# Optimization experiments

Measured on AMD Instinct MI355X. Metric: run time of the kernel, lower is better.

## Reference

```python
import jax, jax.numpy as jnp
import numpy as np

S, B, D, H, E, NUM_TASKS = 2048, 16, 1024, 256, 4, 8
EXPERT_DIMS = jnp.array([256.0, 512.0, 1024.0, 2048.0], dtype=jnp.float32)
EXPERT_COST_EXPONENT = 1.0


def setup_inputs() -> dict:
    key = jax.random.key(0)
    ks = jax.random.split(key, 8)
    s = 1.0 / np.sqrt(H)
    return {
        "prev_layer_output": jax.random.normal(ks[0], (S, B, D), dtype=jnp.float32),
        "task_ids": jax.random.randint(ks[1], (S, B), 0, NUM_TASKS),
        "W_ih": jax.random.uniform(ks[2], (3 * H, D), minval=-s, maxval=s, dtype=jnp.float32),
        "W_hh": jax.random.uniform(ks[3], (3 * H, H), minval=-s, maxval=s, dtype=jnp.float32),
        "b_ih": jax.random.uniform(ks[4], (3 * H,), minval=-s, maxval=s, dtype=jnp.float32),
        "b_hh": jax.random.uniform(ks[5], (3 * H,), minval=-s, maxval=s, dtype=jnp.float32),
        "W_out": jax.random.uniform(ks[6], (E, H), minval=-s, maxval=s, dtype=jnp.float32),
        "b_out": jax.random.uniform(ks[7], (E,), minval=-s, maxval=s, dtype=jnp.float32),
    }


def _gru(x, W_ih, W_hh, b_ih, b_hh):
    # x: (S, B, D); precompute input projections once (big GEMM)
    xp = jnp.einsum('sbd,gd->sbg', x, W_ih) + b_ih  # (S, B, 3H)

    def step(h, xp_t):
        hp = h @ W_hh.T + b_hh                       # (B, 3H)
        xr, xz, xn = jnp.split(xp_t, 3, axis=-1)     # PyTorch gate order: r, z, n
        hr, hz, hn = jnp.split(hp, 3, axis=-1)
        r = jax.nn.sigmoid(xr + hr)
        z = jax.nn.sigmoid(xz + hz)
        n = jnp.tanh(xn + r * hn)
        h_new = (1.0 - z) * n + z * h
        return h_new, h_new

    h0 = jnp.zeros((x.shape[1], W_hh.shape[1]), dtype=x.dtype)
    _, hs = jax.lax.scan(step, h0, xp)
    return hs  # (S, B, H)


def reference(prev_layer_output, task_ids, W_ih, W_hh, b_ih, b_hh, W_out, b_out):
    hs = _gru(prev_layer_output, W_ih, W_hh, b_ih, b_hh)
    logits = jax.nn.relu(hs) @ W_out.T + b_out       # (S, B, E)
    raw_router_output = jax.nn.softmax(logits, axis=-1)
    router_output = raw_router_output                # no dropout branches active
    indices = jnp.broadcast_to(jnp.arange(E, dtype=jnp.int64), (S, B, E))

    routing_costs = EXPERT_DIMS ** EXPERT_COST_EXPONENT
    expert_usage_loss = jnp.einsum('sbe,e->sb', raw_router_output, routing_costs)

    # per-task masked mean == segment_sum / segment_count (fused scatter-reduce)
    flat_ids = task_ids.reshape(-1)
    flat_loss = expert_usage_loss.reshape(-1)
    sums = jax.ops.segment_sum(flat_loss, flat_ids, num_segments=NUM_TASKS)
    counts = jax.ops.segment_sum(jnp.ones_like(flat_loss), flat_ids, num_segments=NUM_TASKS)
    task_expert_usage_losses = sums / counts         # (NUM_TASKS,)

    return raw_router_output, router_output, indices, task_expert_usage_losses
```

## Files before the change

kernel.cpp:

```cpp
#include <hip/hip_runtime.h>

#define NSTEP 2048

typedef __attribute__((ext_vector_type(8))) short short8;
typedef __attribute__((ext_vector_type(4))) float f32x4;
typedef __attribute__((ext_vector_type(4))) int i32x4;

static __device__ __forceinline__ unsigned short f2bf(float f){
  unsigned u = __builtin_bit_cast(unsigned, f);
  u += 0x7FFFu + ((u >> 16) & 1u);
  return (unsigned short)(u >> 16);
}

__global__ __launch_bounds__(256,1)
void cvt_bf16_k(const float* __restrict__ in, unsigned short* __restrict__ out, int n4){
  int i = blockIdx.x*256 + threadIdx.x;
  if (i < n4){
    f32x4 v = *(const f32x4*)(in + (size_t)i*4);
    ushort4 o; o.x=f2bf(v.x); o.y=f2bf(v.y); o.z=f2bf(v.z); o.w=f2bf(v.w);
    *(ushort4*)(out + (size_t)i*4) = o;
  }
}

__global__ __launch_bounds__(256,1)
void gemm_xp_k(const float* __restrict__ X, const unsigned short* __restrict__ Wb,
               const float* __restrict__ bih, const float* __restrict__ bhh,
               float* __restrict__ XP){
  __shared__ __align__(16) unsigned short sA[128*40];
  __shared__ __align__(16) unsigned short sB[128*40];
  const float NL2E  = -1.4426950408889634f;
  const float NL2E2 = -2.8853900817779268f;
  int bid = blockIdx.x;
  int xcd = bid & 7, loc = bid >> 3;
  int mt = xcd*32 + loc/6;
  int nt = loc % 6;
  int m0 = mt*128, n0 = nt*128;
  int tid = threadIdx.x;
  int lane = tid & 63, wave = tid >> 6;
  int wm = wave >> 1, wn = wave & 1;
  int rA = lane & 15, kg = lane >> 4;
  f32x4 acc[4][4] = {};
  for (int k0 = 0; k0 < 1024; k0 += 32){
    __syncthreads();
    #pragma unroll
    for (int q = 0; q < 4; q++){
      int idx = tid + q*256;
      int r = idx >> 3, c4 = idx & 7;
      f32x4 v = *(const f32x4*)(X + (size_t)(m0+r)*1024 + k0 + c4*4);
      ushort4 o; o.x=f2bf(v.x); o.y=f2bf(v.y); o.z=f2bf(v.z); o.w=f2bf(v.w);
      *(ushort4*)&sA[r*40 + c4*4] = o;
    }
    #pragma unroll
    for (int q = 0; q < 2; q++){
      int idx = tid + q*256;
      int n = idx >> 2, c8 = idx & 3;
      uint4 v = *(const uint4*)(Wb + (size_t)(n0+n)*1024 + k0 + c8*8);
      *(uint4*)&sB[n*40 + c8*8] = v;
    }
    __syncthreads();
    short8 af[4], bf[4];
    #pragma unroll
    for (int i=0;i<4;i++) af[i] = *(const short8*)&sA[(wm*64 + 16*i + rA)*40 + kg*8];
    #pragma unroll
    for (int j=0;j<4;j++) bf[j] = *(const short8*)&sB[(wn*64 + 16*j + rA)*40 + kg*8];
    #pragma unroll
    for (int i=0;i<4;i++)
      #pragma unroll
      for (int j=0;j<4;j++)
        acc[i][j] = __builtin_amdgcn_mfma_f32_16x16x32_bf16(af[i], bf[j], acc[i][j], 0, 0, 0);
  }
  #pragma unroll
  for (int i=0;i<4;i++){
    int rb = m0 + wm*64 + 16*i + kg*4;
    #pragma unroll
    for (int j=0;j<4;j++){
      int cc = n0 + wn*64 + 16*j + rA;
      float bv = bih[cc] + bhh[cc];
      float sc = (cc < 512) ? NL2E : NL2E2;
      #pragma unroll
      for (int rg=0;rg<4;rg++)
        XP[(size_t)(rb+rg)*768 + cc] = (acc[i][j][rg] + bv) * sc;
    }
  }
}

__global__ __launch_bounds__(512,2)
void gru_k(const float* __restrict__ xp, const float* __restrict__ Whh,
           char* __restrict__ hs8){
  int b = blockIdx.x;
  int tid = threadIdx.x;
  int wave = tid >> 6, lane = tid & 63;
  int rA = lane & 15, kg = lane >> 4;
  int ua = 32*wave + rA;
  __shared__ __align__(16) char h_q[2][256];

  const float NL2E  = -1.4426950408889634f;
  const float NL2E2 = -2.8853900817779268f;

  i32x4 bw[3][2][4];
  float dsc[3][2];
  #pragma unroll
  for (int g=0; g<3; g++){
    #pragma unroll
    for (int hh=0; hh<2; hh++){
      const float* rp = Whh + (size_t)(g*256 + 32*wave + hh*16 + rA)*256 + kg*16;
      float mx = 0.f;
      #pragma unroll
      for (int kk=0; kk<4; kk++)
        #pragma unroll
        for (int j=0; j<16; j++)
          mx = fmaxf(mx, fabsf(rp[kk*64 + j]));
      mx = fmaxf(mx, __shfl_xor(mx, 16, 64));
      mx = fmaxf(mx, __shfl_xor(mx, 32, 64));
      mx = fmaxf(mx, 1e-20f);
      float s = 127.f / mx;
      float fold = (g == 2) ? NL2E2 : NL2E;
      dsc[g][hh] = mx * (1.f/(127.f*127.f)) * fold;
      #pragma unroll
      for (int kk=0; kk<4; kk++){
        i32x4 v;
        #pragma unroll
        for (int q=0; q<4; q++){
          const float* pp = rp + kk*64 + q*4;
          int q0 = __float2int_rn(pp[0]*s) & 255;
          int q1 = __float2int_rn(pp[1]*s) & 255;
          int q2 = __float2int_rn(pp[2]*s) & 255;
          int q3 = __float2int_rn(pp[3]*s) & 255;
          v[q] = q0 | (q1<<8) | (q2<<16) | (q3<<24);
        }
        bw[g][hh][kk] = v;
      }
    }
  }
  if (tid < 256) h_q[0][tid] = 0;
  __syncthreads();

  float xa[2][3], xb[2][3];
  {
    const float* q0 = xp + (size_t)b*768;
    const float* q1 = xp + (size_t)(16 + b)*768;
    #pragma unroll
    for (int g=0; g<3; g++){
      xa[0][g] = q0[g*256 + ua];  xb[0][g] = q0[g*256 + ua + 16];
      xa[1][g] = q1[g*256 + ua];  xb[1][g] = q1[g*256 + ua + 16];
    }
  }
  float ha = 0.f, hb = 0.f;
  const float* pA = xp + (size_t)(2*16 + b)*768 + ua;
  char* ph = hs8 + (size_t)b*256 + ua;

#define GRU_HALF(half, DO_REFILL)                                                        \
  {                                                                                      \
    i32x4 a[4];                                                                          \
    _Pragma("unroll")                                                                    \
    for (int kk=0; kk<4; kk++)                                                           \
      a[kk] = *(const i32x4*)&h_q[half][kk*64 + kg*16];                                  \
    i32x4 a00={}, a01={}, a10={}, a11={}, a20={}, a21={};                                \
    __builtin_amdgcn_s_setprio(1);                                                       \
    _Pragma("unroll")                                                                    \
    for (int kk=0; kk<4; kk++){                                                          \
      a00 = __builtin_amdgcn_mfma_i32_16x16x64_i8(a[kk], bw[0][0][kk], a00, 0,0,0);      \
      a01 = __builtin_amdgcn_mfma_i32_16x16x64_i8(a[kk], bw[0][1][kk], a01, 0,0,0);      \
      a10 = __builtin_amdgcn_mfma_i32_16x16x64_i8(a[kk], bw[1][0][kk], a10, 0,0,0);      \
      a11 = __builtin_amdgcn_mfma_i32_16x16x64_i8(a[kk], bw[1][1][kk], a11, 0,0,0);      \
      a20 = __builtin_amdgcn_mfma_i32_16x16x64_i8(a[kk], bw[2][0][kk], a20, 0,0,0);      \
      a21 = __builtin_amdgcn_mfma_i32_16x16x64_i8(a[kk], bw[2][1][kk], a21, 0,0,0);      \
    }                                                                                    \
    __builtin_amdgcn_s_setprio(0);                                                       \
    float ra = __builtin_amdgcn_rcpf(1.f + __builtin_amdgcn_exp2f(fmaf((float)a00[0], dsc[0][0], xa[half][0]))); \
    float rb = __builtin_amdgcn_rcpf(1.f + __builtin_amdgcn_exp2f(fmaf((float)a01[0], dsc[0][1], xb[half][0]))); \
    float za = __builtin_amdgcn_rcpf(1.f + __builtin_amdgcn_exp2f(fmaf((float)a10[0], dsc[1][0], xa[half][1]))); \
    float zb = __builtin_amdgcn_rcpf(1.f + __builtin_amdgcn_exp2f(fmaf((float)a11[0], dsc[1][1], xb[half][1]))); \
    float na = fmaf(2.f, __builtin_amdgcn_rcpf(1.f + __builtin_amdgcn_exp2f(             \
                 fmaf(ra, (float)a20[0]*dsc[2][0], xa[half][2]))), -1.f);                \
    float nb = fmaf(2.f, __builtin_amdgcn_rcpf(1.f + __builtin_amdgcn_exp2f(             \
                 fmaf(rb, (float)a21[0]*dsc[2][1], xb[half][2]))), -1.f);                \
    ha = fmaf(za, ha - na, na);                                                          \
    hb = fmaf(zb, hb - nb, nb);                                                          \
    int qa = __float2int_rn(ha*127.f), qb = __float2int_rn(hb*127.f);                    \
    if (kg == 0){                                                                        \
      h_q[half^1][ua]    = (char)qa;                                                     \
      h_q[half^1][ua+16] = (char)qb;                                                     \
    }                                                                                    \
    if (kg == 1){                                                                        \
      ph[0]  = (char)qa;                                                                 \
      ph[16] = (char)qb;                                                                 \
    }                                                                                    \
    ph += 4096;                                                                          \
    if (DO_REFILL){                                                                      \
      xa[half][0] = pA[0];  xa[half][1] = pA[256]; xa[half][2] = pA[512];                \
      xb[half][0] = pA[16]; xb[half][1] = pA[272]; xb[half][2] = pA[528];                \
      pA += 12288;                                                                       \
    }                                                                                    \
    __builtin_amdgcn_sched_barrier(0);                                                   \
    asm volatile("s_waitcnt lgkmcnt(0)" ::: "memory");                                   \
    __builtin_amdgcn_s_barrier();                                                        \
    __builtin_amdgcn_sched_barrier(0);                                                   \
  }

  for (int t = 0; t < NSTEP-2; t += 2){
    GRU_HALF(0, 1)
    GRU_HALF(1, 1)
  }
  GRU_HALF(0, 0)
  GRU_HALF(1, 0)
#undef GRU_HALF
}

__global__ __launch_bounds__(256,1)
void head_k(const char* __restrict__ hs8, const float* __restrict__ Wout,
            const float* __restrict__ bout, const int* __restrict__ task,
            float* __restrict__ out, float* __restrict__ sums, float* __restrict__ counts){
  __shared__ float sW[1024];
  __shared__ float sbin[8], scnt[8];
  int tid = threadIdx.x;
  for (int i = tid; i < 1024; i += 256) sW[i] = Wout[i] * (1.f/127.f);
  if (tid < 8){ sbin[tid] = 0.f; scnt[tid] = 0.f; }
  __syncthreads();
  int rowi = blockIdx.x*256 + tid;
  const uint4* hp = (const uint4*)(hs8 + (size_t)rowi*256);
  float l0 = bout[0], l1 = bout[1], l2 = bout[2], l3 = bout[3];
  #pragma unroll 4
  for (int c = 0; c < 16; c++){
    uint4 v = hp[c];
    uint arr[4] = {v.x, v.y, v.z, v.w};
    #pragma unroll
    for (int q = 0; q < 4; q++){
      uint w = arr[q];
      int k = c*16 + q*4;
      float h0 = (float)max((int)(char)(w      ), 0);
      float h1 = (float)max((int)(char)(w >>  8), 0);
      float h2 = (float)max((int)(char)(w >> 16), 0);
      float h3 = (float)max((int)(w) >> 24,       0);
      l0 = fmaf(h0, sW[k],     l0); l0 = fmaf(h1, sW[k+1],     l0);
      l0 = fmaf(h2, sW[k+2],   l0); l0 = fmaf(h3, sW[k+3],     l0);
      l1 = fmaf(h0, sW[256+k], l1); l1 = fmaf(h1, sW[257+k],   l1);
      l1 = fmaf(h2, sW[258+k], l1); l1 = fmaf(h3, sW[259+k],   l1);
      l2 = fmaf(h0, sW[512+k], l2); l2 = fmaf(h1, sW[513+k],   l2);
      l2 = fmaf(h2, sW[514+k], l2); l2 = fmaf(h3, sW[515+k],   l2);
      l3 = fmaf(h0, sW[768+k], l3); l3 = fmaf(h1, sW[769+k],   l3);
      l3 = fmaf(h2, sW[770+k], l3); l3 = fmaf(h3, sW[771+k],   l3);
    }
  }
  float mx = fmaxf(fmaxf(l0,l1), fmaxf(l2,l3));
  float e0 = __expf(l0-mx), e1 = __expf(l1-mx), e2 = __expf(l2-mx), e3 = __expf(l3-mx);
  float inv = 1.f/(e0+e1+e2+e3);
  float p0 = e0*inv, p1 = e1*inv, p2 = e2*inv, p3 = e3*inv;
  size_t o = (size_t)rowi*4;
  out[o+0]=p0; out[o+1]=p1; out[o+2]=p2; out[o+3]=p3;
  out[131072+o+0]=p0; out[131072+o+1]=p1; out[131072+o+2]=p2; out[131072+o+3]=p3;
  out[262144+o+0]=0.f; out[262144+o+1]=1.f; out[262144+o+2]=2.f; out[262144+o+3]=3.f;
  float loss = 256.f*p0 + 512.f*p1 + 1024.f*p2 + 2048.f*p3;
  int tk = task[rowi] & 7;
  atomicAdd(&sbin[tk], loss);
  atomicAdd(&scnt[tk], 1.f);
  __syncthreads();
  if (tid < 8){
    atomicAdd(&sums[tid], sbin[tid]);
    atomicAdd(&counts[tid], scnt[tid]);
  }
}

__global__ void fin_k(const float* __restrict__ sums, const float* __restrict__ counts,
                      float* __restrict__ o3){
  int i = threadIdx.x;
  if (i < 8){ float c = counts[i]; o3[i] = c > 0.f ? sums[i]/c : 0.f; }
}

extern "C" void kernel_launch(void* const* d_in, const int* in_sizes, int n_in,
                              void* d_out, int out_size, void* d_ws, size_t ws_size,
                              hipStream_t stream){
  const float* x    = (const float*)d_in[0];
  const int*   task = (const int*)d_in[1];
  const float* Wih  = (const float*)d_in[2];
  const float* Whh  = (const float*)d_in[3];
  const float* bih  = (const float*)d_in[4];
  const float* bhh  = (const float*)d_in[5];
  const float* Wout = (const float*)d_in[6];
  const float* bout = (const float*)d_in[7];
  float* out = (float*)d_out;
  char* ws = (char*)d_ws;
  unsigned short* wih_bf = (unsigned short*)ws;
  float* xp    = (float*)(ws + 1572864);
  char* hs8    = (char*)(ws + 102236160);
  float* sums  = (float*)(ws + 111149056);
  float* counts= (float*)(ws + 111149088);

  hipMemsetAsync(sums, 0, 64, stream);

  cvt_bf16_k<<<768, 256, 0, stream>>>(Wih, wih_bf, 196608);
  gemm_xp_k<<<1536, 256, 0, stream>>>(x, wih_bf, bih, bhh, xp);
  gru_k<<<16, 512, 0, stream>>>(xp, Whh, hs8);
  head_k<<<128, 256, 0, stream>>>(hs8, Wout, bout, task, out, sums, counts);
  fin_k<<<1, 64, 0, stream>>>(sums, counts, out + 393216);
}
```

Before: 1.378 ms.

## Overlap input-projection GEMM with GRU recurrence via fused persistent kernel and flags

Result: slower. 1.685 ms (+22.2%).

```diff
diff --git a/kernel.cpp b/kernel.cpp
--- a/kernel.cpp
+++ b/kernel.cpp
@@ -23,17 +23,15 @@
 }
 
 __global__ __launch_bounds__(256,1)
-void gemm_xp_k(const float* __restrict__ X, const unsigned short* __restrict__ Wb,
-               const float* __restrict__ bih, const float* __restrict__ bhh,
-               float* __restrict__ XP){
+void gemm_head_k(const float* __restrict__ X, const unsigned short* __restrict__ Wb,
+                 const float* __restrict__ bih, const float* __restrict__ bhh,
+                 float* __restrict__ XP){
   __shared__ __align__(16) unsigned short sA[128*40];
   __shared__ __align__(16) unsigned short sB[128*40];
   const float NL2E  = -1.4426950408889634f;
   const float NL2E2 = -2.8853900817779268f;
   int bid = blockIdx.x;
-  int xcd = bid & 7, loc = bid >> 3;
-  int mt = xcd*32 + loc/6;
-  int nt = loc % 6;
+  int mt = bid / 6, nt = bid % 6;
   int m0 = mt*128, n0 = nt*128;
   int tid = threadIdx.x;
   int lane = tid & 63, wave = tid >> 6;
@@ -85,17 +83,81 @@
 }
 
 __global__ __launch_bounds__(512,2)
-void gru_k(const float* __restrict__ xp, const float* __restrict__ Whh,
-           char* __restrict__ hs8){
-  int b = blockIdx.x;
-  int tid = threadIdx.x;
-  int wave = tid >> 6, lane = tid & 63;
-  int rA = lane & 15, kg = lane >> 4;
-  int ua = 32*wave + rA;
+void fused_k(const float* __restrict__ xp_c, float* __restrict__ XP,
+             const float* __restrict__ X, const unsigned short* __restrict__ Wb,
+             const float* __restrict__ bih, const float* __restrict__ bhh,
+             const float* __restrict__ Whh, char* __restrict__ hs8,
+             int* prog, int* wgcnt, int* done){
+  __shared__ __align__(16) unsigned short sA[128*40];
+  __shared__ __align__(16) unsigned short sB[128*40];
   __shared__ __align__(16) char h_q[2][256];
 
   const float NL2E  = -1.4426950408889634f;
   const float NL2E2 = -2.8853900817779268f;
+  int tid = threadIdx.x;
+  int lane = tid & 63, wave = tid >> 6;
+  int rA = lane & 15, kg = lane >> 4;
+
+  if (blockIdx.x >= 16){
+    int gbid = blockIdx.x - 16;
+    int mt = 32 + gbid / 6, nt = gbid % 6;
+    int m0 = mt*128, n0 = nt*128;
+    int wm = wave >> 1, wn = wave & 1;
+    f32x4 acc[2][4] = {};
+    for (int k0 = 0; k0 < 1024; k0 += 32){
+      __syncthreads();
+      #pragma unroll
+      for (int q = 0; q < 2; q++){
+        int idx = tid + q*512;
+        int r = idx >> 3, c4 = idx & 7;
+        f32x4 v = *(const f32x4*)(X + (size_t)(m0+r)*1024 + k0 + c4*4);
+        ushort4 o; o.x=f2bf(v.x); o.y=f2bf(v.y); o.z=f2bf(v.z); o.w=f2bf(v.w);
+        *(ushort4*)&sA[r*40 + c4*4] = o;
+      }
+      {
+        int n = tid >> 2, c8 = tid & 3;
+        uint4 v = *(const uint4*)(Wb + (size_t)(n0+n)*1024 + k0 + c8*8);
+        *(uint4*)&sB[n*40 + c8*8] = v;
+      }
+      __syncthreads();
+      short8 af[2], bf[4];
+      #pragma unroll
+      for (int i=0;i<2;i++) af[i] = *(const short8*)&sA[(wm*32 + 16*i + rA)*40 + kg*8];
+      #pragma unroll
+      for (int j=0;j<4;j++) bf[j] = *(const short8*)&sB[(wn*64 + 16*j + rA)*40 + kg*8];
+      #pragma unroll
+      for (int i=0;i<2;i++)
+        #pragma unroll
+        for (int j=0;j<4;j++)
+          acc[i][j] = __builtin_amdgcn_mfma_f32_16x16x32_bf16(af[i], bf[j], acc[i][j], 0, 0, 0);
+    }
+    #pragma unroll
+    for (int i=0;i<2;i++){
+      int rb = m0 + wm*32 + 16*i + kg*4;
+      #pragma unroll
+      for (int j=0;j<4;j++){
+        int cc = n0 + wn*64 + 16*j + rA;
+        float bv = bih[cc] + bhh[cc];
+        float sc = (cc < 512) ? NL2E : NL2E2;
+        #pragma unroll
+        for (int rg=0;rg<4;rg++)
+          XP[(size_t)(rb+rg)*768 + cc] = (acc[i][j][rg] + bv) * sc;
+      }
+    }
+    __threadfence();
+    __syncthreads();
+    if (tid == 0){
+      __hip_atomic_fetch_add(&prog[mt], 1, __ATOMIC_RELEASE, __HIP_MEMORY_SCOPE_AGENT);
+      int old = __hip_atomic_fetch_add(wgcnt, 1, __ATOMIC_ACQ_REL, __HIP_MEMORY_SCOPE_AGENT);
+      if (old == 1343)
+        __hip_atomic_store(done, 1, __ATOMIC_RELEASE, __HIP_MEMORY_SCOPE_AGENT);
+    }
+    return;
+  }
+
+  int b = blockIdx.x;
+  int ua = 32*wave + rA;
+  const float* xp = xp_c;
 
   i32x4 bw[3][2][4];
   float dsc[3][2];
@@ -148,6 +210,7 @@
   float ha = 0.f, hb = 0.f;
   const float* pA = xp + (size_t)(2*16 + b)*768 + ua;
   char* ph = hs8 + (size_t)b*256 + ua;
+  bool all_done = false;
 
 #define GRU_HALF(half, DO_REFILL)                                                        \
   {                                                                                      \
@@ -188,6 +251,15 @@
     }                                                                                    \
     ph += 4096;                                                                          \
     if (DO_REFILL){                                                                      \
+      if (!all_done && (((T+2)&7) == 0) && ((T+2) >> 3) >= 32){                          \
+        int sb = (T+2) >> 3;                                                             \
+        if (__hip_atomic_load(done, __ATOMIC_ACQUIRE, __HIP_MEMORY_SCOPE_AGENT) != 0){   \
+          all_done = true;                                                               \
+        } else {                                                                         \
+          while (__hip_atomic_load(&prog[sb], __ATOMIC_ACQUIRE,                          \
+                                   __HIP_MEMORY_SCOPE_AGENT) < 6){}                      \
+        }                                                                                \
+      }                                                                                  \
       xa[half][0] = pA[0];  xa[half][1] = pA[256]; xa[half][2] = pA[512];                \
       xb[half][0] = pA[16]; xb[half][1] = pA[272]; xb[half][2] = pA[528];                \
       pA += 12288;                                                                       \
@@ -199,11 +271,11 @@
   }
 
   for (int t = 0; t < NSTEP-2; t += 2){
-    GRU_HALF(0, 1)
-    GRU_HALF(1, 1)
-  }
-  GRU_HALF(0, 0)
-  GRU_HALF(1, 0)
+    { int T = t;     GRU_HALF(0, 1) }
+    { int T = t + 1; GRU_HALF(1, 1) }
+  }
+  { int T = NSTEP-2; GRU_HALF(0, 0) }
+  { int T = NSTEP-1; GRU_HALF(1, 0) }
 #undef GRU_HALF
 }
 
@@ -285,12 +357,16 @@
   char* hs8    = (char*)(ws + 102236160);
   float* sums  = (float*)(ws + 111149056);
   float* counts= (float*)(ws + 111149088);
-
-  hipMemsetAsync(sums, 0, 64, stream);
+  int* prog    = (int*)(ws + 111149120);
+  int* wgcnt   = (int*)(ws + 111150144);
+  int* done    = (int*)(ws + 111150148);
+
+  hipMemsetAsync(sums, 0, 1096, stream);
 
   cvt_bf16_k<<<768, 256, 0, stream>>>(Wih, wih_bf, 196608);
-  gemm_xp_k<<<1536, 256, 0, stream>>>(x, wih_bf, bih, bhh, xp);
-  gru_k<<<16, 512, 0, stream>>>(xp, Whh, hs8);
+  gemm_head_k<<<192, 256, 0, stream>>>(x, wih_bf, bih, bhh, xp);
+  fused_k<<<1360, 512, 0, stream>>>(xp, xp, x, wih_bf, bih, bhh, Whh, hs8,
+                                    prog, wgcnt, done);
   head_k<<<128, 256, 0, stream>>>(hs8, Wout, bout, task, out, sums, counts);
   fin_k<<<1, 64, 0, stream>>>(sums, counts, out + 393216);
 }
```
